# Optimization experiments

Hardware: AMD Instinct MI355X
Metric: run time of the kernel (lower is better)

## Reference

```python
import jax, jax.numpy as jnp
import numpy as np

B, L, H, A = 2, 384, 256, 14  # batch, total residues (binder+target), hidden, atoms/residue


def setup_inputs() -> dict:
    key = jax.random.key(0)
    ks = jax.random.split(key, 8)
    s = 1.0 / np.sqrt(H)
    h = jax.random.normal(ks[0], (B, L, H), jnp.float32)          # encoder output
    X = jax.random.normal(ks[1], (B, L, A, 3), jnp.float32)       # coordinates
    mask = jnp.ones((B, L), jnp.int32)                             # residue validity mask
    Wx_w = jax.random.normal(ks[2], (H, H), jnp.float32) * s
    Wx_b = jnp.zeros((H,), jnp.float32)
    Ux_w = jax.random.normal(ks[3], (H, H), jnp.float32) * s
    Ux_b = jnp.zeros((H,), jnp.float32)
    Tx_w = jax.random.normal(ks[4], (A, H), jnp.float32) * s
    Tx_b = jnp.zeros((A,), jnp.float32)
    return dict(h=h, X=X, mask=mask, Wx_w=Wx_w, Wx_b=Wx_b,
                Ux_w=Ux_w, Ux_b=Ux_b, Tx_w=Tx_w, Tx_b=Tx_b)


def reference(h, X, mask, Wx_w, Wx_b, Ux_w, Ux_b, Tx_w, Tx_b):
    # One recurrent coordinate-update step of FADocker._forward.
    m = mask.astype(h.dtype)                                   # (B, L)
    hw = h @ Wx_w.T + Wx_b                                     # (B, L, H)  = W_x(h)
    hu = h @ Ux_w.T + Ux_b                                     # (B, L, H)  = U_x(h)
    mij = hw[:, :, None, :] + hu[:, None, :, :]                # (B, L, L, H)
    gate = jnp.einsum('bijh,ah->bija', jax.nn.relu(mij), Tx_w) + Tx_b  # (B, L, L, A) = T_x(mij)
    xij = (X[:, :, None] - X[:, None, :]) * gate[..., None]   # (B, L, L, A, 3)
    f = jnp.einsum('bijac,bj->biac', xij, m)                   # masked sum over j
    f = f / (1e-6 + m.sum(axis=1)[:, None, None, None])        # (B, L, A, 3)
    return X + jnp.clip(f, -20.0, 20.0)
```

## Files before the change

kernel.cpp:

```cpp
#include <hip/hip_runtime.h>
#include <hip/hip_fp16.h>

#define HDIM 256
#define LDIM 384
#define BDIM 2
#define ADIM 14

typedef __attribute__((ext_vector_type(8))) _Float16 f16x8;
typedef __attribute__((ext_vector_type(2))) _Float16 f16x2;
typedef __attribute__((ext_vector_type(4))) float f32x4;

static __device__ __forceinline__ unsigned pack_f16(float x, float y) {
    f16x2 t = {(_Float16)x, (_Float16)y};
    union { f16x2 v; unsigned u; } c; c.v = t;
    return c.u;
}

static __device__ __forceinline__ unsigned relu_add(unsigned a, unsigned b) {
    union { unsigned u; f16x2 v; } ua, ub, ur;
    ua.u = a; ub.u = b;
    const f16x2 z = {(_Float16)0.f, (_Float16)0.f};
    ur.v = __builtin_elementwise_max(ua.v + ub.v, z);
    return ur.u;
}

__global__ __launch_bounds__(256) void k_front(
    const float* __restrict__ h,
    const float* __restrict__ Wx_w, const float* __restrict__ Wx_b,
    const float* __restrict__ Ux_w, const float* __restrict__ Ux_b,
    const float* __restrict__ Tx_w,
    unsigned* __restrict__ hwP, unsigned* __restrict__ huP,
    unsigned* __restrict__ txP)
{
    const int tid = threadIdx.x;
    if (blockIdx.x == 384) {
        for (int idx = tid; idx < 16 * 128; idx += 256) {
            const int a = idx >> 7, k2 = idx & 127;
            unsigned v = 0;
            if (a < ADIM) {
                const float2 tw = *(const float2*)&Tx_w[a * HDIM + 2 * k2];
                v = pack_f16(tw.x, tw.y);
            }
            txP[idx] = v;
        }
        return;
    }
    const int w = tid >> 6, lane = tid & 63;
    const int n = lane & 15, quad = lane >> 4;
    const int g = blockIdx.x * 4 + w;
    const int ctile = g & 31;
    const int rtile = g >> 5;

    const int arow = (ctile & 15) * 16 + n;
    const float* __restrict__ Arow = (ctile < 16) ? &Wx_w[arow * HDIM]
                                                  : &Ux_w[arow * HDIM];
    const float* __restrict__ Brow = &h[(rtile * 16 + n) * HDIM];

    f32x4 acc = {0.f, 0.f, 0.f, 0.f};
    #pragma unroll
    for (int kc = 0; kc < 8; ++kc) {
        const int ko = kc * 32 + quad * 8;
        const float4 a0 = *(const float4*)&Arow[ko];
        const float4 a1 = *(const float4*)&Arow[ko + 4];
        const float4 b0 = *(const float4*)&Brow[ko];
        const float4 b1 = *(const float4*)&Brow[ko + 4];
        union { unsigned u[4]; f16x8 v; } af, bf;
        af.u[0] = pack_f16(a0.x, a0.y); af.u[1] = pack_f16(a0.z, a0.w);
        af.u[2] = pack_f16(a1.x, a1.y); af.u[3] = pack_f16(a1.z, a1.w);
        bf.u[0] = pack_f16(b0.x, b0.y); bf.u[1] = pack_f16(b0.z, b0.w);
        bf.u[2] = pack_f16(b1.x, b1.y); bf.u[3] = pack_f16(b1.z, b1.w);
        acc = __builtin_amdgcn_mfma_f32_16x16x32_f16(af.v, bf.v, acc, 0, 0, 0);
    }

    const int row = rtile * 16 + n;
    const int c0 = (ctile & 15) * 16 + quad * 4;
    const float4 bias = (ctile < 16) ? *(const float4*)&Wx_b[c0]
                                     : *(const float4*)&Ux_b[c0];
    uint2 pv;
    pv.x = pack_f16(acc[0] + bias.x, acc[1] + bias.y);
    pv.y = pack_f16(acc[2] + bias.z, acc[3] + bias.w);
    unsigned* __restrict__ dst = (ctile < 16) ? hwP : huP;
    *(uint2*)&dst[row * 128 + (ctile & 15) * 8 + quad * 2] = pv;
}

__global__ __launch_bounds__(384) void k_main(
    const unsigned* __restrict__ hwP, const unsigned* __restrict__ huP,
    const unsigned* __restrict__ txP,
    const float* __restrict__ X, const int* __restrict__ mask,
    const float* __restrict__ Tx_b,
    float* __restrict__ out)
{
    __shared__ float m_lds[LDIM];
    __shared__ float part2[24 * 16 * 4];
    __shared__ float part_m[24];

    const int i = blockIdx.x, b = blockIdx.y;
    const int tid = threadIdx.x;
    const int w = tid >> 6, lane = tid & 63;
    const int n = lane & 15, quad = lane >> 4;

    m_lds[tid] = (float)mask[b * LDIM + tid];
    __syncthreads();

    const unsigned* __restrict__ hwr = &hwP[(b * LDIM + i) * 128];
    const unsigned* __restrict__ hub = &huP[b * LDIM * 128];
    const unsigned* __restrict__ txr = &txP[n * 128];

    f32x4 acc[4];
    #pragma unroll
    for (int t = 0; t < 4; ++t) acc[t] = (f32x4){0.f, 0.f, 0.f, 0.f};

    #pragma unroll 4
    for (int kc = 0; kc < 8; ++kc) {
        const int ko = kc * 16 + quad * 4;
        const uint4 hw4 = *(const uint4*)&hwr[ko];
        const uint4 tx4 = *(const uint4*)&txr[ko];
        union { unsigned u[4]; f16x8 v; } bfrag;
        bfrag.u[0] = tx4.x; bfrag.u[1] = tx4.y;
        bfrag.u[2] = tx4.z; bfrag.u[3] = tx4.w;
        #pragma unroll
        for (int t = 0; t < 4; ++t) {
            const int j = (w * 4 + t) * 16 + n;
            const uint4 hu4 = *(const uint4*)&hub[j * 128 + ko];
            union { unsigned u[4]; f16x8 v; } af;
            af.u[0] = relu_add(hw4.x, hu4.x);
            af.u[1] = relu_add(hw4.y, hu4.y);
            af.u[2] = relu_add(hw4.z, hu4.z);
            af.u[3] = relu_add(hw4.w, hu4.w);
            acc[t] = __builtin_amdgcn_mfma_f32_16x16x32_f16(af.v, bfrag.v, acc[t], 0, 0, 0);
        }
    }

    float s1 = 0.f, s2x = 0.f, s2y = 0.f, s2z = 0.f, pm = 0.f;
    if (n < ADIM) {
        const float txb = Tx_b[n];
        #pragma unroll
        for (int t = 0; t < 4; ++t) {
            #pragma unroll
            for (int r = 0; r < 4; ++r) {
                const int jd = (w * 4 + t) * 16 + quad * 4 + r;
                const float m = m_lds[jd];
                const float g = acc[t][r] + txb;
                const float mg = m * g;
                const float* __restrict__ Xp = &X[((b * LDIM + jd) * ADIM + n) * 3];
                s1 += mg;
                s2x = fmaf(mg, Xp[0], s2x);
                s2y = fmaf(mg, Xp[1], s2y);
                s2z = fmaf(mg, Xp[2], s2z);
                pm += m;
            }
        }
    }
    {
        f32x4 sv = {s2x, s2y, s2z, s1};
        *(f32x4*)&part2[((w * 4 + quad) * 16 + n) * 4] = sv;
    }
    if (n == 0) part_m[w * 4 + quad] = pm;
    __syncthreads();

    if (tid < 42) {
        const int a = tid / 3, c = tid % 3;
        float S2 = 0.f, S1 = 0.f, msum = 0.f;
        #pragma unroll 4
        for (int g = 0; g < 24; ++g) {
            const float* __restrict__ p = &part2[(g * 16 + a) * 4];
            S2 += p[c]; S1 += p[3]; msum += part_m[g];
        }
        const float denom = 1e-6f + msum;
        const int idx = ((b * LDIM + i) * ADIM + a) * 3 + c;
        const float xi = X[idx];
        float f = (xi * S1 - S2) / denom;
        f = fminf(fmaxf(f, -20.f), 20.f);
        out[idx] = xi + f;
    }
}

extern "C" void kernel_launch(void* const* d_in, const int* in_sizes, int n_in,
                              void* d_out, int out_size, void* d_ws, size_t ws_size,
                              hipStream_t stream) {
    (void)in_sizes; (void)n_in; (void)out_size; (void)ws_size;
    const float* h    = (const float*)d_in[0];
    const float* X    = (const float*)d_in[1];
    const int*   mask = (const int*)  d_in[2];
    const float* Wx_w = (const float*)d_in[3];
    const float* Wx_b = (const float*)d_in[4];
    const float* Ux_w = (const float*)d_in[5];
    const float* Ux_b = (const float*)d_in[6];
    const float* Tx_w = (const float*)d_in[7];
    const float* Tx_b = (const float*)d_in[8];
    float* out = (float*)d_out;

    unsigned* hwP = (unsigned*)d_ws;
    unsigned* huP = hwP + BDIM * LDIM * (HDIM / 2);
    unsigned* txP = huP + BDIM * LDIM * (HDIM / 2);

    k_front<<<385, 256, 0, stream>>>(h, Wx_w, Wx_b, Ux_w, Ux_b, Tx_w, hwP, huP, txP);
    k_main<<<dim3(LDIM, BDIM), 384, 0, stream>>>(hwP, huP, txP, X, mask, Tx_b, out);
}
```

Baseline: 102.0 us.

## Process two query residues per block and stage X coordinates in LDS

Each k_main block now handles two i rows, so every loaded hu fragment and tx fragment feeds two MFMAs and the grid is halved. The batch's full X slice (about 64KB) is copied into shared memory once per block and replaces the scattered global X reads in the epilogue. The cost is more accumulator registers, a large LDS footprint that may limit occupancy, and a per-block X copy repeated across 192 blocks.

```diff
diff --git a/kernel.cpp b/kernel.cpp
--- a/kernel.cpp
+++ b/kernel.cpp
@@ -90,30 +90,42 @@
     const float* __restrict__ Tx_b,
     float* __restrict__ out)
 {
+    __shared__ float Xl[LDIM * 42];
     __shared__ float m_lds[LDIM];
-    __shared__ float part2[24 * 16 * 4];
+    __shared__ float part2[2][24 * 16 * 4];
     __shared__ float part_m[24];
 
-    const int i = blockIdx.x, b = blockIdx.y;
+    const int i0 = blockIdx.x * 2, i1 = i0 + 1;
+    const int b  = blockIdx.y;
     const int tid = threadIdx.x;
     const int w = tid >> 6, lane = tid & 63;
     const int n = lane & 15, quad = lane >> 4;
 
-    m_lds[tid] = (float)mask[b * LDIM + tid];
+    {
+        const float4* __restrict__ Xg4 = (const float4*)&X[b * (LDIM * 42)];
+        float4* __restrict__ Xl4 = (float4*)Xl;
+        for (int idx = tid; idx < LDIM * 42 / 4; idx += 384) Xl4[idx] = Xg4[idx];
+        m_lds[tid] = (float)mask[b * LDIM + tid];
+    }
     __syncthreads();
 
-    const unsigned* __restrict__ hwr = &hwP[(b * LDIM + i) * 128];
-    const unsigned* __restrict__ hub = &huP[b * LDIM * 128];
-    const unsigned* __restrict__ txr = &txP[n * 128];
-
-    f32x4 acc[4];
+    const unsigned* __restrict__ hwr0 = &hwP[(b * LDIM + i0) * 128];
+    const unsigned* __restrict__ hwr1 = &hwP[(b * LDIM + i1) * 128];
+    const unsigned* __restrict__ hub  = &huP[b * LDIM * 128];
+    const unsigned* __restrict__ txr  = &txP[n * 128];
+
+    f32x4 acc0[4], acc1[4];
     #pragma unroll
-    for (int t = 0; t < 4; ++t) acc[t] = (f32x4){0.f, 0.f, 0.f, 0.f};
-
-    #pragma unroll 4
+    for (int t = 0; t < 4; ++t) {
+        acc0[t] = (f32x4){0.f, 0.f, 0.f, 0.f};
+        acc1[t] = (f32x4){0.f, 0.f, 0.f, 0.f};
+    }
+
+    #pragma unroll 2
     for (int kc = 0; kc < 8; ++kc) {
         const int ko = kc * 16 + quad * 4;
-        const uint4 hw4 = *(const uint4*)&hwr[ko];
+        const uint4 hwa = *(const uint4*)&hwr0[ko];
+        const uint4 hwb = *(const uint4*)&hwr1[ko];
         const uint4 tx4 = *(const uint4*)&txr[ko];
         union { unsigned u[4]; f16x8 v; } bfrag;
         bfrag.u[0] = tx4.x; bfrag.u[1] = tx4.y;
@@ -123,55 +135,66 @@
             const int j = (w * 4 + t) * 16 + n;
             const uint4 hu4 = *(const uint4*)&hub[j * 128 + ko];
             union { unsigned u[4]; f16x8 v; } af;
-            af.u[0] = relu_add(hw4.x, hu4.x);
-            af.u[1] = relu_add(hw4.y, hu4.y);
-            af.u[2] = relu_add(hw4.z, hu4.z);
-            af.u[3] = relu_add(hw4.w, hu4.w);
-            acc[t] = __builtin_amdgcn_mfma_f32_16x16x32_f16(af.v, bfrag.v, acc[t], 0, 0, 0);
-        }
-    }
-
-    float s1 = 0.f, s2x = 0.f, s2y = 0.f, s2z = 0.f, pm = 0.f;
-    if (n < ADIM) {
-        const float txb = Tx_b[n];
-        #pragma unroll
-        for (int t = 0; t < 4; ++t) {
+            af.u[0] = relu_add(hwa.x, hu4.x);
+            af.u[1] = relu_add(hwa.y, hu4.y);
+            af.u[2] = relu_add(hwa.z, hu4.z);
+            af.u[3] = relu_add(hwa.w, hu4.w);
+            acc0[t] = __builtin_amdgcn_mfma_f32_16x16x32_f16(af.v, bfrag.v, acc0[t], 0, 0, 0);
+            af.u[0] = relu_add(hwb.x, hu4.x);
+            af.u[1] = relu_add(hwb.y, hu4.y);
+            af.u[2] = relu_add(hwb.z, hu4.z);
+            af.u[3] = relu_add(hwb.w, hu4.w);
+            acc1[t] = __builtin_amdgcn_mfma_f32_16x16x32_f16(af.v, bfrag.v, acc1[t], 0, 0, 0);
+        }
+    }
+
+    float pm = 0.f;
+    #pragma unroll
+    for (int ii = 0; ii < 2; ++ii) {
+        const f32x4* acc = ii ? acc1 : acc0;
+        float s1 = 0.f, s2x = 0.f, s2y = 0.f, s2z = 0.f;
+        if (n < ADIM) {
+            const float txb = Tx_b[n];
             #pragma unroll
-            for (int r = 0; r < 4; ++r) {
-                const int jd = (w * 4 + t) * 16 + quad * 4 + r;
-                const float m = m_lds[jd];
-                const float g = acc[t][r] + txb;
-                const float mg = m * g;
-                const float* __restrict__ Xp = &X[((b * LDIM + jd) * ADIM + n) * 3];
-                s1 += mg;
-                s2x = fmaf(mg, Xp[0], s2x);
-                s2y = fmaf(mg, Xp[1], s2y);
-                s2z = fmaf(mg, Xp[2], s2z);
-                pm += m;
+            for (int t = 0; t < 4; ++t) {
+                #pragma unroll
+                for (int r = 0; r < 4; ++r) {
+                    const int jd = (w * 4 + t) * 16 + quad * 4 + r;
+                    const float m = m_lds[jd];
+                    const float g = acc[t][r] + txb;
+                    const float mg = m * g;
+                    const float* __restrict__ Xp = &Xl[jd * 42 + n * 3];
+                    s1 += mg;
+                    s2x = fmaf(mg, Xp[0], s2x);
+                    s2y = fmaf(mg, Xp[1], s2y);
+                    s2z = fmaf(mg, Xp[2], s2z);
+                    if (ii == 0) pm += m;
+                }
             }
         }
-    }
-    {
         f32x4 sv = {s2x, s2y, s2z, s1};
-        *(f32x4*)&part2[((w * 4 + quad) * 16 + n) * 4] = sv;
+        *(f32x4*)&part2[ii][((w * 4 + quad) * 16 + n) * 4] = sv;
     }
     if (n == 0) part_m[w * 4 + quad] = pm;
     __syncthreads();
 
-    if (tid < 42) {
-        const int a = tid / 3, c = tid % 3;
+    int ii = -1, t42 = 0;
+    if (tid < 42)                    { ii = 0; t42 = tid; }
+    else if (tid >= 64 && tid < 106) { ii = 1; t42 = tid - 64; }
+    if (ii >= 0) {
+        const int a = t42 / 3, c = t42 % 3;
+        const int i = ii ? i1 : i0;
         float S2 = 0.f, S1 = 0.f, msum = 0.f;
         #pragma unroll 4
         for (int g = 0; g < 24; ++g) {
-            const float* __restrict__ p = &part2[(g * 16 + a) * 4];
+            const float* __restrict__ p = &part2[ii][(g * 16 + a) * 4];
             S2 += p[c]; S1 += p[3]; msum += part_m[g];
         }
         const float denom = 1e-6f + msum;
-        const int idx = ((b * LDIM + i) * ADIM + a) * 3 + c;
-        const float xi = X[idx];
+        const float xi = Xl[i * 42 + t42];
         float f = (xi * S1 - S2) / denom;
         f = fminf(fmaxf(f, -20.f), 20.f);
-        out[idx] = xi + f;
+        out[((b * LDIM + i) * ADIM + a) * 3 + c] = xi + f;
     }
 }
 
@@ -195,5 +218,5 @@
     unsigned* txP = huP + BDIM * LDIM * (HDIM / 2);
 
     k_front<<<385, 256, 0, stream>>>(h, Wx_w, Wx_b, Ux_w, Ux_b, Tx_w, hwP, huP, txP);
-    k_main<<<dim3(LDIM, BDIM), 384, 0, stream>>>(hwP, huP, txP, X, mask, Tx_b, out);
-}
+    k_main<<<dim3(LDIM / 2, BDIM), 384, 0, stream>>>(hwP, huP, txP, X, mask, Tx_b, out);
+}
```

Measured after the change: 101.4 us. Within noise of the previous version (-0.6%).
